# Kernel tuning notes

Measured on AMD Instinct MI355X. Metric: run time of the kernel, lower is better.

## Reference

```python
import jax, jax.numpy as jnp
import numpy as np

NUM_STEPS = 16  # step_index values in [0, 16); step 0 is excluded from pooling
BETA = 0.1
EPS = 1e-8


def setup_inputs() -> dict:
    key = jax.random.key(0)
    k1, k2, k3, k4, k5 = jax.random.split(key, 5)
    B, N, T, H, D = 8, 8, 2048, 2048, 1
    return {
        "policy_responses_logps": jax.random.normal(k1, (B, N, T, D), dtype=jnp.float32),
        "reference_responses_logps": jax.random.normal(k2, (B, N, T, D), dtype=jnp.float32),
        "hidden_state": jax.random.normal(k3, (B, N, T, H), dtype=jnp.float32),
        "step_index": jax.random.randint(k4, (B, N, T), 0, NUM_STEPS, dtype=jnp.int32),
        "labels": jax.random.normal(k5, (B, N), dtype=jnp.float32),
    }


def _segment_stats(onehot, x, counts):
    # onehot: [B,N,T,S], x: [B,N,T,F] -> per-step mean [B,N,S,F]
    ssum = jnp.einsum('bnts,bntf->bnsf', onehot, x)
    return ssum / jnp.maximum(counts, 1.0)[..., None]


def _lambda_rank_loss(pred, labels):
    # pred, labels: [B,N]
    N = pred.shape[1]
    diff = pred[:, :, None] - pred[:, None, :]            # [B,N,N]
    label_diff = labels[:, :, None] - labels[:, None, :]
    pairwise = -jax.nn.log_sigmoid(diff * jnp.sign(label_diff))
    return (pairwise.sum(axis=(1, 2)) / (N * (N - 1))).mean()


def reference(policy_responses_logps, reference_responses_logps, hidden_state, step_index, labels):
    logits = policy_responses_logps - reference_responses_logps  # [B,N,T,D]

    onehot = jax.nn.one_hot(step_index, NUM_STEPS, dtype=hidden_state.dtype)  # [B,N,T,S]
    counts = onehot.sum(axis=2)                                               # [B,N,S]

    step_hidden = _segment_stats(onehot, hidden_state, counts)  # [B,N,S,H]
    ref_hidden = step_hidden[:, 0:1]                             # [B,1,S,H]

    # cosine similarity between each (b,n,s) step-mean and the reference (n=0) step-mean
    dot = jnp.einsum('bnsh,bosh->bns', step_hidden, ref_hidden)
    nrm = jnp.maximum(jnp.linalg.norm(step_hidden, axis=-1), EPS)        # [B,N,S]
    ref_nrm = jnp.maximum(jnp.linalg.norm(ref_hidden, axis=-1), EPS)      # [B,1,S]
    cos = dot / (nrm * ref_nrm)

    s_ids = jnp.arange(NUM_STEPS)
    valid = (counts > 0) & (counts[:, 0:1] > 0) & (s_ids >= 1)[None, None, :]
    step_weights = jnp.where(valid, cos + 1.0, 0.0)                        # [B,N,S]

    step_logit = _segment_stats(onehot, logits, counts)                    # [B,N,S,D]
    weighted_sum = jnp.einsum('bns,bnsd->bnd', step_weights, step_logit)
    total_weight = step_weights.sum(axis=-1)                               # [B,N]
    weighted_logits = jnp.where(total_weight[..., None] > 0,
                                weighted_sum / jnp.maximum(total_weight, EPS)[..., None],
                                0.0)                                       # [B,N,D]

    text_logits = weighted_logits.mean(axis=-1)                            # [B,N]
    lr = _lambda_rank_loss(text_logits, labels)
    loss = -jax.nn.log_sigmoid(BETA * lr)

    chosen_rewards = (policy_responses_logps[:, 0, :] - reference_responses_logps[:, 0, :]).mean()
    rejected_rewards = (policy_responses_logps[:, -1, :] - reference_responses_logps[:, -1, :]).mean()
    return (loss, chosen_rewards, rejected_rewards)
```

## Files before the change

kernel.cpp:

```cpp
#include <hip/hip_runtime.h>
#include <math.h>

#define TT 2048
#define HH 2048
#define NSTEP 16
#define EPSF 1e-8f
#define BETA 0.1f
#define TSPLIT 4
#define TCHUNK (TT / TSPLIT)
#define ROW2 (HH / 2)
#define PART_FLOATS ((size_t)64 * NSTEP * HH)

__global__ __launch_bounds__(256, 4) void k_segsum2(const float* __restrict__ hidden,
                                                    const int* __restrict__ step,
                                                    float2* __restrict__ part) {
  const int bn   = blockIdx.y;
  const int z    = blockIdx.z;
  const int col2 = blockIdx.x * 256 + threadIdx.x;
  const int t0   = z * TCHUNK;

  __shared__ int s_step[TCHUNK];
  for (int i = threadIdx.x; i < TCHUNK; i += 256) s_step[i] = step[bn * TT + t0 + i];
  __syncthreads();

  const float2* hp = (const float2*)hidden + (size_t)(bn * TT + t0) * ROW2 + col2;

  float2 acc[NSTEP];
#pragma unroll
  for (int k = 0; k < NSTEP; ++k) acc[k] = make_float2(0.f, 0.f);

  float2 va[8], vb[8];
  int4 sa0, sa1, sb0, sb1;

#define LOADS(S0, S1, base)                         \
  { S0 = *(const int4*)&s_step[(base)];             \
    S1 = *(const int4*)&s_step[(base) + 4]; }

#define LOADG(dst, base)                                        \
  _Pragma("unroll")                                             \
  for (int u = 0; u < 8; ++u) dst[u] = hp[(size_t)((base) + u) * ROW2];

#define ACC1(V, SS)                                                            \
  { const int s_ = __builtin_amdgcn_readfirstlane(SS);                         \
    switch (s_) {                                                              \
      case 0:  acc[0].x  += V.x; acc[0].y  += V.y; break;                      \
      case 1:  acc[1].x  += V.x; acc[1].y  += V.y; break;                      \
      case 2:  acc[2].x  += V.x; acc[2].y  += V.y; break;                      \
      case 3:  acc[3].x  += V.x; acc[3].y  += V.y; break;                      \
      case 4:  acc[4].x  += V.x; acc[4].y  += V.y; break;                      \
      case 5:  acc[5].x  += V.x; acc[5].y  += V.y; break;                      \
      case 6:  acc[6].x  += V.x; acc[6].y  += V.y; break;                      \
      case 7:  acc[7].x  += V.x; acc[7].y  += V.y; break;                      \
      case 8:  acc[8].x  += V.x; acc[8].y  += V.y; break;                      \
      case 9:  acc[9].x  += V.x; acc[9].y  += V.y; break;                      \
      case 10: acc[10].x += V.x; acc[10].y += V.y; break;                      \
      case 11: acc[11].x += V.x; acc[11].y += V.y; break;                      \
      case 12: acc[12].x += V.x; acc[12].y += V.y; break;                      \
      case 13: acc[13].x += V.x; acc[13].y += V.y; break;                      \
      case 14: acc[14].x += V.x; acc[14].y += V.y; break;                      \
      case 15: acc[15].x += V.x; acc[15].y += V.y; break;                      \
    } }

#define PROC(src, S0, S1)                                                      \
  ACC1(src[0], S0.x) ACC1(src[1], S0.y) ACC1(src[2], S0.z) ACC1(src[3], S0.w) \
  ACC1(src[4], S1.x) ACC1(src[5], S1.y) ACC1(src[6], S1.z) ACC1(src[7], S1.w)

  LOADS(sa0, sa1, 0)
  LOADG(va, 0)
  for (int t = 0; t < TCHUNK; t += 16) {
    LOADS(sb0, sb1, t + 8)
    LOADG(vb, t + 8)
    PROC(va, sa0, sa1)
    if (t + 16 < TCHUNK) { LOADS(sa0, sa1, t + 16) LOADG(va, t + 16) }
    PROC(vb, sb0, sb1)
  }
#undef LOADS
#undef LOADG
#undef ACC1
#undef PROC

  float2* op = (float2*)part + (size_t)z * (PART_FLOATS / 2) +
               ((size_t)bn * NSTEP) * ROW2 + col2;
#pragma unroll
  for (int k = 0; k < NSTEP; ++k) op[(size_t)k * ROW2] = acc[k];
}

__global__ __launch_bounds__(256) void k_reduce(const float4* __restrict__ part,
                                                float4* __restrict__ ssum) {
  const size_t i = (size_t)blockIdx.x * 256 + threadIdx.x;
  const size_t slice = PART_FLOATS / 4;
  float4 s = part[i];
#pragma unroll
  for (int zz = 1; zz < TSPLIT; ++zz) {
    const float4 v = part[(size_t)zz * slice + i];
    s.x += v.x; s.y += v.y; s.z += v.z; s.w += v.w;
  }
  ssum[i] = s;
}

__global__ __launch_bounds__(1024) void k_bn(const float* __restrict__ pol,
                                             const float* __restrict__ refp,
                                             const int* __restrict__ step,
                                             const float* __restrict__ ssum,
                                             float* __restrict__ text_logits) {
  const int bn  = blockIdx.x;
  const int b   = bn >> 3;
  const int bn0 = b << 3;
  const int wave = threadIdx.x >> 6;
  const int lane = threadIdx.x & 63;

  __shared__ float cnt[NSTEP], cnt0[NSTEP], lsum[NSTEP], wgt[NSTEP];
  if (threadIdx.x < NSTEP) {
    cnt[threadIdx.x] = 0.f; cnt0[threadIdx.x] = 0.f; lsum[threadIdx.x] = 0.f;
  }
  __syncthreads();

  for (int t = threadIdx.x; t < TT; t += 1024) {
    const int s = step[bn * TT + t];
    atomicAdd(&cnt[s], 1.f);
    atomicAdd(&lsum[s], pol[bn * TT + t] - refp[bn * TT + t]);
    const int s0 = step[bn0 * TT + t];
    atomicAdd(&cnt0[s0], 1.f);
  }
  __syncthreads();

  const int s = wave;
  const float c  = fmaxf(cnt[s],  1.f);
  const float c0 = fmaxf(cnt0[s], 1.f);
  const float ic  = 1.f / c;
  const float ic0 = 1.f / c0;
  const float4* p  = (const float4*)(ssum + ((size_t)bn  * NSTEP + s) * HH);
  const float4* p0 = (const float4*)(ssum + ((size_t)bn0 * NSTEP + s) * HH);

  float dot = 0.f, nn = 0.f, rr = 0.f;
#pragma unroll
  for (int i = 0; i < 8; ++i) {
    const float4 a4 = p[lane + i * 64];
    const float4 r4 = p0[lane + i * 64];
    const float ax = a4.x * ic, ay = a4.y * ic, az = a4.z * ic, aw = a4.w * ic;
    const float rx = r4.x * ic0, ry = r4.y * ic0, rz = r4.z * ic0, rw = r4.w * ic0;
    dot += ax * rx + ay * ry + az * rz + aw * rw;
    nn  += ax * ax + ay * ay + az * az + aw * aw;
    rr  += rx * rx + ry * ry + rz * rz + rw * rw;
  }
#pragma unroll
  for (int off = 32; off > 0; off >>= 1) {
    dot += __shfl_down(dot, off);
    nn  += __shfl_down(nn,  off);
    rr  += __shfl_down(rr,  off);
  }
  if (lane == 0) {
    const float nrm = fmaxf(sqrtf(nn), EPSF);
    const float rn  = fmaxf(sqrtf(rr), EPSF);
    const float cosv = dot / (nrm * rn);
    const bool valid = (cnt[s] > 0.f) && (cnt0[s] > 0.f) && (s >= 1);
    wgt[s] = valid ? (cosv + 1.f) : 0.f;
  }
  __syncthreads();

  if (threadIdx.x == 0) {
    float wsum = 0.f, tw = 0.f;
#pragma unroll
    for (int k = 0; k < NSTEP; ++k) {
      const float w = wgt[k];
      wsum += w * (lsum[k] / fmaxf(cnt[k], 1.f));
      tw   += w;
    }
    text_logits[bn] = (tw > 0.f) ? (wsum / fmaxf(tw, EPSF)) : 0.f;
  }
}

__device__ inline float softplus_f(float x) {
  return fmaxf(x, 0.f) + log1pf(expf(-fabsf(x)));
}

__global__ __launch_bounds__(256) void k_final(const float* __restrict__ pol,
                                               const float* __restrict__ refp,
                                               const float* __restrict__ labels,
                                               const float* __restrict__ text_logits,
                                               float* __restrict__ out) {
  const int which = blockIdx.x;
  const int wave = threadIdx.x >> 6;
  const int lane = threadIdx.x & 63;
  __shared__ float red[4];

  if (which == 0) {
    float part = 0.f;
    if (threadIdx.x < 64) {
      const int b = threadIdx.x >> 3, i = threadIdx.x & 7;
      const float pi = text_logits[b * 8 + i];
      const float li = labels[b * 8 + i];
#pragma unroll
      for (int j = 0; j < 8; ++j) {
        const float ld = li - labels[b * 8 + j];
        const float sg = (ld > 0.f) ? 1.f : ((ld < 0.f) ? -1.f : 0.f);
        const float z  = (pi - text_logits[b * 8 + j]) * sg;
        part += softplus_f(-z);
      }
    }
    if (wave == 0) {
#pragma unroll
      for (int off = 32; off > 0; off >>= 1) part += __shfl_down(part, off);
      if (lane == 0) {
        const float lr = part / (56.f * 8.f);
        out[0] = softplus_f(-BETA * lr);
      }
    }
  } else {
    const int n = (which == 1) ? 0 : 7;
    float s = 0.f;
    for (int i = threadIdx.x; i < 8 * TT; i += 256) {
      const int b = i >> 11, t = i & (TT - 1);
      const size_t idx = ((size_t)(b * 8 + n)) * TT + t;
      s += pol[idx] - refp[idx];
    }
#pragma unroll
    for (int off = 32; off > 0; off >>= 1) s += __shfl_down(s, off);
    if (lane == 0) red[wave] = s;
    __syncthreads();
    if (threadIdx.x == 0)
      out[which] = (red[0] + red[1] + red[2] + red[3]) / (8.f * TT);
  }
}

extern "C" void kernel_launch(void* const* d_in, const int* in_sizes, int n_in,
                              void* d_out, int out_size, void* d_ws, size_t ws_size,
                              hipStream_t stream) {
  const float* pol    = (const float*)d_in[0];
  const float* refp   = (const float*)d_in[1];
  const float* hidden = (const float*)d_in[2];
  const int*   step   = (const int*)d_in[3];
  const float* labels = (const float*)d_in[4];
  float* out = (float*)d_out;

  float* part = (float*)d_ws;
  float* ssum = part + (size_t)TSPLIT * PART_FLOATS;
  float* text_logits = ssum + PART_FLOATS;

  dim3 g1(4, 64, TSPLIT);
  k_segsum2<<<g1, 256, 0, stream>>>(hidden, step, (float2*)part);
  k_reduce<<<(int)(PART_FLOATS / 4 / 256), 256, 0, stream>>>((const float4*)part,
                                                             (float4*)ssum);
  k_bn<<<64, 1024, 0, stream>>>(pol, refp, step, ssum, text_logits);
  k_final<<<3, 256, 0, stream>>>(pol, refp, labels, text_logits, out);
}
```

Measured before the change: 251.3 us.

## Fold T-split partial reduction into k_bn and halve the T split

Cuts the time split of the segment-sum kernel from 4 to 2 and removes the separate reduce kernel. k_bn now adds the two partial sums as it reads them. It also gives each wave its own shared-memory histogram to reduce atomic contention. The aim is to drop one launch plus the partial-buffer write and reread traffic. The cost is half as many blocks in the segment-sum kernel (1024 → 512), which may lower occupancy on a 256-CU device.

```diff
diff --git a/kernel.cpp b/kernel.cpp
--- a/kernel.cpp
+++ b/kernel.cpp
@@ -6,7 +6,7 @@
 #define NSTEP 16
 #define EPSF 1e-8f
 #define BETA 0.1f
-#define TSPLIT 4
+#define TSPLIT 2
 #define TCHUNK (TT / TSPLIT)
 #define ROW2 (HH / 2)
 #define PART_FLOATS ((size_t)64 * NSTEP * HH)
@@ -85,23 +85,10 @@
   for (int k = 0; k < NSTEP; ++k) op[(size_t)k * ROW2] = acc[k];
 }
 
-__global__ __launch_bounds__(256) void k_reduce(const float4* __restrict__ part,
-                                                float4* __restrict__ ssum) {
-  const size_t i = (size_t)blockIdx.x * 256 + threadIdx.x;
-  const size_t slice = PART_FLOATS / 4;
-  float4 s = part[i];
-#pragma unroll
-  for (int zz = 1; zz < TSPLIT; ++zz) {
-    const float4 v = part[(size_t)zz * slice + i];
-    s.x += v.x; s.y += v.y; s.z += v.z; s.w += v.w;
-  }
-  ssum[i] = s;
-}
-
 __global__ __launch_bounds__(1024) void k_bn(const float* __restrict__ pol,
                                              const float* __restrict__ refp,
                                              const int* __restrict__ step,
-                                             const float* __restrict__ ssum,
+                                             const float* __restrict__ part,
                                              float* __restrict__ text_logits) {
   const int bn  = blockIdx.x;
   const int b   = bn >> 3;
@@ -109,18 +96,32 @@
   const int wave = threadIdx.x >> 6;
   const int lane = threadIdx.x & 63;
 
+  __shared__ float cnt_w[16][NSTEP], lsum_w[16][NSTEP], cnt0_w[16][NSTEP];
   __shared__ float cnt[NSTEP], cnt0[NSTEP], lsum[NSTEP], wgt[NSTEP];
-  if (threadIdx.x < NSTEP) {
-    cnt[threadIdx.x] = 0.f; cnt0[threadIdx.x] = 0.f; lsum[threadIdx.x] = 0.f;
+
+  if (lane < NSTEP) {
+    cnt_w[wave][lane] = 0.f; lsum_w[wave][lane] = 0.f; cnt0_w[wave][lane] = 0.f;
   }
   __syncthreads();
 
   for (int t = threadIdx.x; t < TT; t += 1024) {
     const int s = step[bn * TT + t];
-    atomicAdd(&cnt[s], 1.f);
-    atomicAdd(&lsum[s], pol[bn * TT + t] - refp[bn * TT + t]);
+    atomicAdd(&cnt_w[wave][s], 1.f);
+    atomicAdd(&lsum_w[wave][s], pol[bn * TT + t] - refp[bn * TT + t]);
     const int s0 = step[bn0 * TT + t];
-    atomicAdd(&cnt0[s0], 1.f);
+    atomicAdd(&cnt0_w[wave][s0], 1.f);
+  }
+  __syncthreads();
+
+  if (threadIdx.x < NSTEP) {
+    float c = 0.f, l = 0.f, c0 = 0.f;
+#pragma unroll
+    for (int w = 0; w < 16; ++w) {
+      c  += cnt_w[w][threadIdx.x];
+      l  += lsum_w[w][threadIdx.x];
+      c0 += cnt0_w[w][threadIdx.x];
+    }
+    cnt[threadIdx.x] = c; lsum[threadIdx.x] = l; cnt0[threadIdx.x] = c0;
   }
   __syncthreads();
 
@@ -129,16 +130,21 @@
   const float c0 = fmaxf(cnt0[s], 1.f);
   const float ic  = 1.f / c;
   const float ic0 = 1.f / c0;
-  const float4* p  = (const float4*)(ssum + ((size_t)bn  * NSTEP + s) * HH);
-  const float4* p0 = (const float4*)(ssum + ((size_t)bn0 * NSTEP + s) * HH);
+  const float4* po0 = (const float4*)(part + ((size_t)bn  * NSTEP + s) * HH);
+  const float4* po1 = (const float4*)(part + PART_FLOATS + ((size_t)bn  * NSTEP + s) * HH);
+  const float4* pr0 = (const float4*)(part + ((size_t)bn0 * NSTEP + s) * HH);
+  const float4* pr1 = (const float4*)(part + PART_FLOATS + ((size_t)bn0 * NSTEP + s) * HH);
 
   float dot = 0.f, nn = 0.f, rr = 0.f;
 #pragma unroll
   for (int i = 0; i < 8; ++i) {
-    const float4 a4 = p[lane + i * 64];
-    const float4 r4 = p0[lane + i * 64];
-    const float ax = a4.x * ic, ay = a4.y * ic, az = a4.z * ic, aw = a4.w * ic;
-    const float rx = r4.x * ic0, ry = r4.y * ic0, rz = r4.z * ic0, rw = r4.w * ic0;
+    const int idx = lane + i * 64;
+    const float4 a0 = po0[idx], a1 = po1[idx];
+    const float4 r0 = pr0[idx], r1 = pr1[idx];
+    const float ax = (a0.x + a1.x) * ic,  ay = (a0.y + a1.y) * ic;
+    const float az = (a0.z + a1.z) * ic,  aw = (a0.w + a1.w) * ic;
+    const float rx = (r0.x + r1.x) * ic0, ry = (r0.y + r1.y) * ic0;
+    const float rz = (r0.z + r1.z) * ic0, rw = (r0.w + r1.w) * ic0;
     dot += ax * rx + ay * ry + az * rz + aw * rw;
     nn  += ax * ax + ay * ay + az * az + aw * aw;
     rr  += rx * rx + ry * ry + rz * rz + rw * rw;
@@ -234,13 +240,10 @@
   float* out = (float*)d_out;
 
   float* part = (float*)d_ws;
-  float* ssum = part + (size_t)TSPLIT * PART_FLOATS;
-  float* text_logits = ssum + PART_FLOATS;
+  float* text_logits = part + (size_t)TSPLIT * PART_FLOATS;
 
   dim3 g1(4, 64, TSPLIT);
   k_segsum2<<<g1, 256, 0, stream>>>(hidden, step, (float2*)part);
-  k_reduce<<<(int)(PART_FLOATS / 4 / 256), 256, 0, stream>>>((const float4*)part,
-                                                             (float4*)ssum);
-  k_bn<<<64, 1024, 0, stream>>>(pol, refp, step, ssum, text_logits);
+  k_bn<<<64, 1024, 0, stream>>>(pol, refp, step, part, text_logits);
   k_final<<<3, 256, 0, stream>>>(pol, refp, labels, text_logits, out);
 }
```

Result: faster. 238.8 us (-5.0%).
